# Performance work log

Hardware: AMD Instinct MI355X
Metric: run time of the kernel (lower is better)

Reference implementation:

```python
import jax, jax.numpy as jnp
import numpy as np

B, E, L, H = 4, 1024, 2048, 16
DH = E // H
SCALE = E ** -0.5  # note: original scales by embedding_dim**-0.5, not head_dim**-0.5


def setup_inputs() -> dict:
    key = jax.random.key(0)
    k1, k2, k3 = jax.random.split(key, 3)
    x = jax.random.normal(k1, (B, E, L), dtype=jnp.float32)
    # Linear init: randn(d_in, d_out) / d_in
    W_qkv = jax.random.normal(k2, (E, E), dtype=jnp.float32) / E
    W_proj = jax.random.normal(k3, (E, E), dtype=jnp.float32) / E
    b_proj = jnp.zeros((E,), dtype=jnp.float32)
    return {"x": x, "W_qkv": W_qkv, "W_proj": W_proj, "b_proj": b_proj}


def reference(x, W_qkv, W_proj, b_proj):
    b, e, l = x.shape
    # shared Q=K=V projection (channels-first Linear: (x^T @ M)^T)
    kqv = jnp.einsum('bel,ef->bfl', x, W_qkv)            # [B, E, L]
    kqv = kqv.reshape(b, H, DH, l)                        # [B, H, Dh, L]
    # scores[b,h,i,j] = <kqv[...,i], kqv[...,j]> over head dim
    scores = jnp.einsum('bhdi,bhdj->bhij', kqv, kqv)      # [B, H, L, L]
    # mask strictly-lower triangle (i > j), then scale; softmax over query axis (-2)
    mask = jnp.tril(jnp.ones((l, l), dtype=bool), k=-1)
    scores = jnp.where(mask, -jnp.inf, scores * SCALE)
    att = jax.nn.softmax(scores, axis=-2)                 # normalize over i (rows)
    # t[...,d,j] = sum_i kqv[...,d,i] * att[...,i,j]
    t = jnp.einsum('bhdi,bhij->bhdj', kqv, att).reshape(b, e, l)
    # output projection with bias (dropout is identity in eval)
    out = jnp.einsum('bel,ef->bfl', t, W_proj) + b_proj[None, :, None]
    return out
```

## Files before the change

kernel.cpp:

```cpp
#include <hip/hip_runtime.h>
#include <stdint.h>
#include <math.h>

#define B_ 4
#define E_ 1024
#define L_ 2048
#define H_ 16
#define DH_ 64
#define SCALE_ 0.03125f

typedef __bf16 bf16;
typedef __bf16 bf16x8 __attribute__((ext_vector_type(8)));
typedef __bf16 bf16x4 __attribute__((ext_vector_type(4)));
typedef float f32x4 __attribute__((ext_vector_type(4)));

__device__ __forceinline__ f32x4 mfma16(bf16x8 a, bf16x8 b, f32x4 c) {
  return __builtin_amdgcn_mfma_f32_16x16x32_bf16(a, b, c, 0, 0, 0);
}

__device__ __forceinline__ void gl_lds16(const void* g, void* lds) {
  auto* lp = reinterpret_cast<__attribute__((address_space(3))) unsigned int*>(
      reinterpret_cast<uintptr_t>(lds));
  const auto* gp = reinterpret_cast<const __attribute__((address_space(1))) unsigned int*>(
      reinterpret_cast<uintptr_t>(g));
  __builtin_amdgcn_global_load_lds(gp, lp, 16, 0, 0);
}

__global__ __launch_bounds__(256) void tconv(const float* __restrict__ in,
                                             bf16* __restrict__ out, int R, int C) {
  in  += (size_t)blockIdx.z * R * C;
  out += (size_t)blockIdx.z * R * C;
  __shared__ float t[32][33];
  const int r0 = blockIdx.x * 32, c0 = blockIdx.y * 32;
  const int lx = threadIdx.x & 31, ly = threadIdx.x >> 5;
#pragma unroll
  for (int q = 0; q < 4; q++)
    t[ly + q * 8][lx] = in[(size_t)(r0 + ly + q * 8) * C + c0 + lx];
  __syncthreads();
#pragma unroll
  for (int q = 0; q < 4; q++) {
    int c = ly + q * 8;
    out[(size_t)(c0 + c) * R + r0 + lx] = (bf16)t[lx][c];
  }
}

__global__ __launch_bounds__(256) void wconv(const float* __restrict__ in0,
                                             const float* __restrict__ in1,
                                             bf16* __restrict__ out0,
                                             bf16* __restrict__ out1) {
  const float* in = blockIdx.z ? in1 : in0;
  bf16* out = blockIdx.z ? out1 : out0;
  __shared__ float t[32][33];
  const int r0 = blockIdx.x * 32, c0 = blockIdx.y * 32;
  const int lx = threadIdx.x & 31, ly = threadIdx.x >> 5;
#pragma unroll
  for (int q = 0; q < 4; q++)
    t[ly + q * 8][lx] = in[(size_t)(r0 + ly + q * 8) * E_ + c0 + lx];
  __syncthreads();
#pragma unroll
  for (int q = 0; q < 4; q++) {
    int c = ly + q * 8;
    out[(size_t)(c0 + c) * E_ + r0 + lx] = (bf16)t[lx][c];
  }
}

template <int EPI>
__global__ __launch_bounds__(256) void gemm_bt(const bf16* __restrict__ A,
                                               const bf16* __restrict__ Bt,
                                               bf16* __restrict__ outT,
                                               bf16* __restrict__ outD,
                                               float* __restrict__ outF,
                                               const float* __restrict__ bias) {
  constexpr int M = E_, N = L_, K = E_;
  constexpr int NIT = K / 32;
  const int bm = blockIdx.x, bn = blockIdx.y, b = blockIdx.z;
  __shared__ bf16 As[3][128 * 32];
  __shared__ bf16 Bs[3][128 * 32];
  const int tid = threadIdx.x, w = tid >> 6, l = tid & 63;
  const int wm = (w >> 1) << 6, wn = (w & 1) << 6;
  const bf16* Ap = A + (size_t)bm * 128 * K;
  const bf16* Bp = Bt + (size_t)b * N * K + (size_t)bn * 128 * K;
  f32x4 acc[4][4] = {};
  const int g0 = (w * 2 + 0) * 64 + l, g1 = (w * 2 + 1) * 64 + l;
  const int r0 = g0 >> 2, s0 = (g0 & 3) ^ ((r0 >> 1) & 3);
  const int r1 = g1 >> 2, s1 = (g1 & 3) ^ ((r1 >> 1) & 3);

#define STAGE_G(kt_, buf)                                              \
  do {                                                                 \
    gl_lds16(Ap + (size_t)r0 * K + (kt_) + s0 * 8, &As[buf][g0 * 8]);  \
    gl_lds16(Ap + (size_t)r1 * K + (kt_) + s1 * 8, &As[buf][g1 * 8]);  \
    gl_lds16(Bp + (size_t)r0 * K + (kt_) + s0 * 8, &Bs[buf][g0 * 8]);  \
    gl_lds16(Bp + (size_t)r1 * K + (kt_) + s1 * 8, &Bs[buf][g1 * 8]);  \
  } while (0)

  STAGE_G(0, 0);
  STAGE_G(32, 1);
  asm volatile("s_waitcnt vmcnt(4)" ::: "memory");
  __builtin_amdgcn_s_barrier();
#pragma unroll 1
  for (int it = 0; it < NIT; it++) {
    const int cur = it - (it / 3) * 3;
    if (it + 2 < NIT) STAGE_G((it + 2) * 32, (it + 2) - ((it + 2) / 3) * 3);
    bf16x8 af[4], bfr[4];
#pragma unroll
    for (int fm = 0; fm < 4; fm++) {
      int row = wm + fm * 16 + (l & 15);
      int gg = row * 4 + ((l >> 4) ^ ((row >> 1) & 3));
      af[fm] = *(const bf16x8*)(&As[cur][gg * 8]);
    }
#pragma unroll
    for (int fn = 0; fn < 4; fn++) {
      int row = wn + fn * 16 + (l & 15);
      int gg = row * 4 + ((l >> 4) ^ ((row >> 1) & 3));
      bfr[fn] = *(const bf16x8*)(&Bs[cur][gg * 8]);
    }
#pragma unroll
    for (int fm = 0; fm < 4; fm++)
#pragma unroll
      for (int fn = 0; fn < 4; fn++)
        acc[fm][fn] = mfma16(af[fm], bfr[fn], acc[fm][fn]);
    if (it + 2 < NIT) {
      asm volatile("s_waitcnt vmcnt(4)" ::: "memory");
    } else if (it + 1 < NIT) {
      asm volatile("s_waitcnt vmcnt(0)" ::: "memory");
    }
    __builtin_amdgcn_s_barrier();
  }
#undef STAGE_G
  const int cm = bm * 128 + wm, cn = bn * 128 + wn;
  if (EPI == 0) {
#pragma unroll
    for (int fn = 0; fn < 4; fn++) {
#pragma unroll
      for (int fm = 0; fm < 4; fm++) {
        int n = cn + fn * 16 + (l & 15);
        int m = cm + fm * 16 + ((l >> 4) << 2);
        f32x4 v = acc[fm][fn];
        bf16x4 pv = {(bf16)v[0], (bf16)v[1], (bf16)v[2], (bf16)v[3]};
        *(bf16x4*)(outT + (size_t)b * N * M + (size_t)n * M + m) = pv;
#pragma unroll
        for (int r = 0; r < 4; r++)
          outD[(size_t)b * M * N + (size_t)(m + r) * N + n] = pv[r];
      }
    }
  } else {
#pragma unroll
    for (int fm = 0; fm < 4; fm++) {
      int m = cm + fm * 16 + ((l >> 4) << 2);
#pragma unroll
      for (int r = 0; r < 4; r++) {
        float bv = bias[m + r];
#pragma unroll
        for (int fn = 0; fn < 4; fn++) {
          int n = cn + fn * 16 + (l & 15);
          outF[(size_t)b * M * N + (size_t)(m + r) * N + n] = acc[fm][fn][r] + bv;
        }
      }
    }
  }
}

__global__ __launch_bounds__(512) void attn(const bf16* __restrict__ kqvT,
                                            const bf16* __restrict__ kqvD,
                                            bf16* __restrict__ tT) {
  const int linear = (int)blockIdx.x + 16 * ((int)blockIdx.y + 16 * (int)blockIdx.z);
  const int qb = 15 - (linear >> 6);
  const int h = linear & 15, b = (linear >> 4) & 3;
  const int tid = threadIdx.x, w = tid >> 6, l = tid & 63;
  const int j0 = qb * 128 + w * 16;
  __shared__ bf16 Ks[2][64 * 64];
  __shared__ bf16 Vs[2][64 * 64];
  __shared__ bf16 Ps[8][16 * 64];
  const size_t bT = (size_t)b * L_ * E_;
  const size_t bD = (size_t)b * E_ * L_;
  bf16x8 qa[2];
  {
    size_t qoff = bT + (size_t)(j0 + (l & 15)) * E_ + h * 64 + ((l >> 4) << 3);
    qa[0] = *(const bf16x8*)(kqvT + qoff);
    qa[1] = *(const bf16x8*)(kqvT + qoff + 32);
#pragma unroll
    for (int e = 0; e < 8; e++) {
      qa[0][e] = (bf16)((float)qa[0][e] * SCALE_);
      qa[1][e] = (bf16)((float)qa[1][e] * SCALE_);
    }
  }
  float mrun[4] = {0.f, 0.f, 0.f, 0.f};
  float lsum[4] = {0.f, 0.f, 0.f, 0.f};
  f32x4 tacc[4] = {};
  bf16* myPs = &Ps[w][0];
  const int g = w * 64 + l;
  const int rS = g >> 3, sS = (g & 7) ^ (rS & 7);
  const int nch = 2 * (qb + 1);

#define STAGE(c, buf)                                                                  \
  do {                                                                                 \
    const int i0_ = (c) * 64;                                                          \
    gl_lds16(kqvT + bT + (size_t)(i0_ + rS) * E_ + h * 64 + sS * 8, &Ks[buf][g * 8]);  \
    gl_lds16(kqvD + bD + (size_t)(h * 64 + rS) * L_ + i0_ + sS * 8, &Vs[buf][g * 8]);  \
  } while (0)

  STAGE(0, 0);
  asm volatile("s_waitcnt vmcnt(0)" ::: "memory");
  __syncthreads();

#pragma unroll 1
  for (int c = 0; c < nch; c++) {
    const int cur = c & 1;
    if (c + 1 < nch) STAGE(c + 1, cur ^ 1);
    const int i0 = c * 64;
    const bf16* Kc = &Ks[cur][0];
    const bf16* Vc = &Vs[cur][0];
    if (i0 <= j0 + 15) {
      f32x4 sacc[4];
      __builtin_amdgcn_s_setprio(1);
#pragma unroll
      for (int fi = 0; fi < 4; fi++) {
        int row = fi * 16 + (l & 15);
        bf16x8 k0 = *(const bf16x8*)(Kc + row * 64 + (((l >> 4) ^ (row & 7)) << 3));
        bf16x8 k1 = *(const bf16x8*)(Kc + row * 64 + ((((l >> 4) + 4) ^ (row & 7)) << 3));
        f32x4 z = {};
        z = mfma16(qa[0], k0, z);
        z = mfma16(qa[1], k1, z);
        sacc[fi] = z;
      }
      __builtin_amdgcn_s_setprio(0);
      const int jrb = j0 + ((l >> 4) << 2);
      if (i0 + 63 > j0) {
#pragma unroll
        for (int fi = 0; fi < 4; fi++) {
          int i = i0 + fi * 16 + (l & 15);
#pragma unroll
          for (int r = 0; r < 4; r++)
            if (i > jrb + r) sacc[fi][r] = -INFINITY;
        }
      }
      bool ov = false;
#pragma unroll
      for (int fi = 0; fi < 4; fi++)
#pragma unroll
        for (int r = 0; r < 4; r++) ov |= (sacc[fi][r] > mrun[r] + 8.f);
      if (__any(ov)) {
        float mx[4];
#pragma unroll
        for (int r = 0; r < 4; r++)
          mx[r] = fmaxf(fmaxf(sacc[0][r], sacc[1][r]), fmaxf(sacc[2][r], sacc[3][r]));
#pragma unroll
        for (int r = 0; r < 4; r++) {
          mx[r] = fmaxf(mx[r], __shfl_xor(mx[r], 1));
          mx[r] = fmaxf(mx[r], __shfl_xor(mx[r], 2));
          mx[r] = fmaxf(mx[r], __shfl_xor(mx[r], 4));
          mx[r] = fmaxf(mx[r], __shfl_xor(mx[r], 8));
        }
#pragma unroll
        for (int r = 0; r < 4; r++) {
          float mn = fmaxf(mrun[r], mx[r]);
          float a = __expf(mrun[r] - mn);
          lsum[r] *= a;
#pragma unroll
          for (int fd = 0; fd < 4; fd++) tacc[fd][r] *= a;
          mrun[r] = mn;
        }
      }
#pragma unroll
      for (int fi = 0; fi < 4; fi++) {
        int icol = fi * 16 + (l & 15);
#pragma unroll
        for (int r = 0; r < 4; r++) {
          float p = __expf(sacc[fi][r] - mrun[r]);
          lsum[r] += p;
          int jl = ((l >> 4) << 2) + r;
          int slot = (icol >> 3) ^ (jl & 7);
          myPs[jl * 64 + slot * 8 + (icol & 7)] = (bf16)p;
        }
      }
      bf16x8 pa[2];
      {
        int jl = l & 15;
#pragma unroll
        for (int kc = 0; kc < 2; kc++)
          pa[kc] = *(const bf16x8*)(myPs + jl * 64 + (((kc * 4 + (l >> 4)) ^ (jl & 7)) << 3));
      }
      __builtin_amdgcn_s_setprio(1);
#pragma unroll
      for (int fd = 0; fd < 4; fd++) {
        int row = fd * 16 + (l & 15);
#pragma unroll
        for (int kc = 0; kc < 2; kc++) {
          bf16x8 vf = *(const bf16x8*)(Vc + row * 64 + (((kc * 4 + (l >> 4)) ^ (row & 7)) << 3));
          tacc[fd] = mfma16(pa[kc], vf, tacc[fd]);
        }
      }
      __builtin_amdgcn_s_setprio(0);
    }
    asm volatile("s_waitcnt vmcnt(0)" ::: "memory");
    __syncthreads();
  }
#undef STAGE
#pragma unroll
  for (int r = 0; r < 4; r++) {
    lsum[r] += __shfl_xor(lsum[r], 1);
    lsum[r] += __shfl_xor(lsum[r], 2);
    lsum[r] += __shfl_xor(lsum[r], 4);
    lsum[r] += __shfl_xor(lsum[r], 8);
  }
#pragma unroll
  for (int r = 0; r < 4; r++) {
    int j = j0 + ((l >> 4) << 2) + r;
    float inv = 1.0f / lsum[r];
#pragma unroll
    for (int fd = 0; fd < 4; fd++) {
      int d = fd * 16 + (l & 15);
      tT[bT + (size_t)j * E_ + h * 64 + d] = (bf16)(tacc[fd][r] * inv);
    }
  }
}

extern "C" void kernel_launch(void* const* d_in, const int* in_sizes, int n_in,
                              void* d_out, int out_size, void* d_ws, size_t ws_size,
                              hipStream_t stream) {
  const float* x     = (const float*)d_in[0];
  const float* Wqkv  = (const float*)d_in[1];
  const float* Wproj = (const float*)d_in[2];
  const float* bias  = (const float*)d_in[3];
  float* out = (float*)d_out;
  char* ws = (char*)d_ws;
  bf16* Wt_qkv  = (bf16*)ws;
  bf16* Wt_proj = (bf16*)(ws + (2ull << 20));
  bf16* xT      = (bf16*)(ws + (4ull << 20));
  bf16* kqvT    = (bf16*)(ws + (20ull << 20));
  bf16* kqvD    = (bf16*)(ws + (36ull << 20));
  bf16* tT      = xT;

  wconv<<<dim3(32, 32, 2), 256, 0, stream>>>(Wqkv, Wproj, Wt_qkv, Wt_proj);
  tconv<<<dim3(32, 64, B_), 256, 0, stream>>>(x, xT, E_, L_);
  gemm_bt<0><<<dim3(8, 16, B_), 256, 0, stream>>>(Wt_qkv, xT, kqvT, kqvD,
                                                  (float*)nullptr, (const float*)nullptr);
  attn<<<dim3(16, 16, B_), 512, 0, stream>>>(kqvT, kqvD, tT);
  gemm_bt<1><<<dim3(8, 16, B_), 256, 0, stream>>>(Wt_proj, tT, (bf16*)nullptr,
                                                  (bf16*)nullptr, out, bias);
}
```

Measured before the change: 213.7 us.

## Enlarge GEMM tile to 256x128 with 512 threads, XCD-aware block remap

The projection GEMMs now use 512-thread blocks that each compute a 256x128 output tile over a unified shared-memory buffer, so every B tile loaded from global memory serves twice as many rows. The 1D grid is remapped so that consecutive blocks on the same XCD share the same batch and column panel, which is meant to improve L2 reuse. MFMA sections also raise wave priority with s_setprio. The costs are fewer blocks (256, roughly one per CU) and more LDS per block, which may lower occupancy and latency hiding.

After: 210.9 us. No clear change (-1.3%).

```diff
diff --git a/kernel.cpp b/kernel.cpp
--- a/kernel.cpp
+++ b/kernel.cpp
@@ -65,7 +65,7 @@
 }
 
 template <int EPI>
-__global__ __launch_bounds__(256) void gemm_bt(const bf16* __restrict__ A,
+__global__ __launch_bounds__(512) void gemm_bt(const bf16* __restrict__ A,
                                                const bf16* __restrict__ Bt,
                                                bf16* __restrict__ outT,
                                                bf16* __restrict__ outD,
@@ -73,29 +73,28 @@
                                                const float* __restrict__ bias) {
   constexpr int M = E_, N = L_, K = E_;
   constexpr int NIT = K / 32;
-  const int bm = blockIdx.x, bn = blockIdx.y, b = blockIdx.z;
-  __shared__ bf16 As[3][128 * 32];
-  __shared__ bf16 Bs[3][128 * 32];
+  const int lin = (int)blockIdx.x;
+  const int lgc = (lin & 7) * 32 + (lin >> 3);
+  const int bn = lgc & 15, bm = (lgc >> 4) & 3, b = lgc >> 6;
+  __shared__ bf16 AB[3][384 * 32];
   const int tid = threadIdx.x, w = tid >> 6, l = tid & 63;
   const int wm = (w >> 1) << 6, wn = (w & 1) << 6;
-  const bf16* Ap = A + (size_t)bm * 128 * K;
+  const bf16* Ap = A + (size_t)bm * 256 * K;
   const bf16* Bp = Bt + (size_t)b * N * K + (size_t)bn * 128 * K;
   f32x4 acc[4][4] = {};
-  const int g0 = (w * 2 + 0) * 64 + l, g1 = (w * 2 + 1) * 64 + l;
-  const int r0 = g0 >> 2, s0 = (g0 & 3) ^ ((r0 >> 1) & 3);
-  const int r1 = g1 >> 2, s1 = (g1 & 3) ^ ((r1 >> 1) & 3);
-
-#define STAGE_G(kt_, buf)                                              \
-  do {                                                                 \
-    gl_lds16(Ap + (size_t)r0 * K + (kt_) + s0 * 8, &As[buf][g0 * 8]);  \
-    gl_lds16(Ap + (size_t)r1 * K + (kt_) + s1 * 8, &As[buf][g1 * 8]);  \
-    gl_lds16(Bp + (size_t)r0 * K + (kt_) + s0 * 8, &Bs[buf][g0 * 8]);  \
-    gl_lds16(Bp + (size_t)r1 * K + (kt_) + s1 * 8, &Bs[buf][g1 * 8]);  \
+  const int rr = tid >> 2, s = (tid & 3) ^ ((rr >> 1) & 3);
+
+#define STAGE_G(kt_, buf)                                                           \
+  do {                                                                              \
+    gl_lds16(Ap + (size_t)rr * K + (kt_) + s * 8, &AB[buf][(size_t)tid * 8]);       \
+    gl_lds16(Ap + (size_t)(rr + 128) * K + (kt_) + s * 8,                           \
+             &AB[buf][(size_t)(tid + 512) * 8]);                                    \
+    gl_lds16(Bp + (size_t)rr * K + (kt_) + s * 8, &AB[buf][(size_t)(tid + 1024) * 8]); \
   } while (0)
 
   STAGE_G(0, 0);
   STAGE_G(32, 1);
-  asm volatile("s_waitcnt vmcnt(4)" ::: "memory");
+  asm volatile("s_waitcnt vmcnt(3)" ::: "memory");
   __builtin_amdgcn_s_barrier();
 #pragma unroll 1
   for (int it = 0; it < NIT; it++) {
@@ -106,28 +105,30 @@
     for (int fm = 0; fm < 4; fm++) {
       int row = wm + fm * 16 + (l & 15);
       int gg = row * 4 + ((l >> 4) ^ ((row >> 1) & 3));
-      af[fm] = *(const bf16x8*)(&As[cur][gg * 8]);
+      af[fm] = *(const bf16x8*)(&AB[cur][gg * 8]);
     }
 #pragma unroll
     for (int fn = 0; fn < 4; fn++) {
-      int row = wn + fn * 16 + (l & 15);
+      int row = 256 + wn + fn * 16 + (l & 15);
       int gg = row * 4 + ((l >> 4) ^ ((row >> 1) & 3));
-      bfr[fn] = *(const bf16x8*)(&Bs[cur][gg * 8]);
-    }
+      bfr[fn] = *(const bf16x8*)(&AB[cur][gg * 8]);
+    }
+    __builtin_amdgcn_s_setprio(1);
 #pragma unroll
     for (int fm = 0; fm < 4; fm++)
 #pragma unroll
       for (int fn = 0; fn < 4; fn++)
         acc[fm][fn] = mfma16(af[fm], bfr[fn], acc[fm][fn]);
+    __builtin_amdgcn_s_setprio(0);
     if (it + 2 < NIT) {
-      asm volatile("s_waitcnt vmcnt(4)" ::: "memory");
+      asm volatile("s_waitcnt vmcnt(3)" ::: "memory");
     } else if (it + 1 < NIT) {
       asm volatile("s_waitcnt vmcnt(0)" ::: "memory");
     }
     __builtin_amdgcn_s_barrier();
   }
 #undef STAGE_G
-  const int cm = bm * 128 + wm, cn = bn * 128 + wn;
+  const int cm = bm * 256 + wm, cn = bn * 128 + wn;
   if (EPI == 0) {
 #pragma unroll
     for (int fn = 0; fn < 4; fn++) {
@@ -333,9 +334,9 @@
 
   wconv<<<dim3(32, 32, 2), 256, 0, stream>>>(Wqkv, Wproj, Wt_qkv, Wt_proj);
   tconv<<<dim3(32, 64, B_), 256, 0, stream>>>(x, xT, E_, L_);
-  gemm_bt<0><<<dim3(8, 16, B_), 256, 0, stream>>>(Wt_qkv, xT, kqvT, kqvD,
+  gemm_bt<0><<<dim3(256, 1, 1), 512, 0, stream>>>(Wt_qkv, xT, kqvT, kqvD,
                                                   (float*)nullptr, (const float*)nullptr);
   attn<<<dim3(16, 16, B_), 512, 0, stream>>>(kqvT, kqvD, tT);
-  gemm_bt<1><<<dim3(8, 16, B_), 256, 0, stream>>>(Wt_proj, tT, (bf16*)nullptr,
+  gemm_bt<1><<<dim3(256, 1, 1), 512, 0, stream>>>(Wt_proj, tT, (bf16*)nullptr,
                                                   (bf16*)nullptr, out, bias);
 }
```
